# Kernel optimization log

Hardware: AMD Instinct MI355X
Metric: run time of the kernel (lower is better)

Reference implementation:

```python
import jax, jax.numpy as jnp
import numpy as np

N = 1024
B = 32768


def _cc_mul(a, b):
    # complex multiply with real/imag stacked on axis 0; b broadcasts [2,N] against [2,B,N]
    real = a[0] * b[0] - a[1] * b[1]
    imag = a[0] * b[1] + a[1] * b[0]
    return jnp.stack((real, imag), axis=0)


def setup_inputs() -> dict:
    key = jax.random.key(0)
    k1, k2, k3, k4, k5 = jax.random.split(key, 5)
    x = jax.random.normal(k1, (2, B, N), dtype=jnp.float32)
    diag = jax.random.normal(k2, (2, N), dtype=jnp.float32)
    off_diag = jax.random.normal(k3, (2, N), dtype=jnp.float32)
    # pairwise swap permutation: (0,1),(2,3),... swapped -> 1,0,3,2,...
    pairwise = np.arange(N).reshape(-1, 2)[:, ::-1].ravel()
    pairwise_perm_idx = jnp.asarray(pairwise, dtype=jnp.int32)
    left_perm_idx = jax.random.permutation(k4, N).astype(jnp.int32)
    right_perm_idx = jax.random.permutation(k5, N).astype(jnp.int32)
    return {
        "x": x,
        "diag": diag,
        "off_diag": off_diag,
        "pairwise_perm_idx": pairwise_perm_idx,
        "left_perm_idx": left_perm_idx,
        "right_perm_idx": right_perm_idx,
    }


def reference(x, diag, off_diag, pairwise_perm_idx, left_perm_idx, right_perm_idx):
    # left permutation (gather on last dim)
    o = x[..., left_perm_idx]
    # diag path + pairwise-permuted off-diag path (complex MAC)
    out = _cc_mul(o, diag) + _cc_mul(o, off_diag)[..., pairwise_perm_idx]
    # right permutation
    return out[..., right_perm_idx]
```

## Files before the change

### kernel.cpp

```cpp
#include <hip/hip_runtime.h>


#define NCOLS 1024
#define TPB   256
#define KPT   (NCOLS / TPB)
#define BPB   8

__global__ __launch_bounds__(TPB) void mesh_kernel(
    const float* __restrict__ x,
    const float* __restrict__ diag,
    const float* __restrict__ offd,
    const int*   __restrict__ pair,
    const int*   __restrict__ lperm,
    const int*   __restrict__ rperm,
    float* __restrict__ out,
    int B)
{
    __shared__ __align__(16) float smem[2][2 * NCOLS];

    const int t = threadIdx.x;

    int   lr[KPT], lp[KPT];
    float d0[KPT], d1[KPT], f0[KPT], f1[KPT];
#pragma unroll
    for (int k = 0; k < KPT; ++k) {
        int j = t + k * TPB;
        int r = rperm[j];
        int p = pair[r];
        lr[k] = lperm[r];
        lp[k] = lperm[p];
        d0[k] = diag[r];
        d1[k] = diag[NCOLS + r];
        f0[k] = offd[p];
        f1[k] = offd[NCOLS + p];
    }

    const long long BN = (long long)B * NCOLS;
    const int b0 = blockIdx.x * BPB;

    for (int i = 0; i < BPB; ++i) {
        int b = b0 + i;
        if (b >= B) break;
        float* sb = smem[i & 1];

        const float4* r0 = (const float4*)(x + (long long)b * NCOLS);
        const float4* r1 = (const float4*)(x + BN + (long long)b * NCOLS);
        ((float4*)sb)[t]           = r0[t];
        ((float4*)(sb + NCOLS))[t] = r1[t];
        __syncthreads();

#pragma unroll
        for (int k = 0; k < KPT; ++k) {
            float a0 = sb[lr[k]];
            float a1 = sb[NCOLS + lr[k]];
            float e0 = sb[lp[k]];
            float e1 = sb[NCOLS + lp[k]];
            int j = t + k * TPB;
            long long o = (long long)b * NCOLS + j;
            out[o]      = a0 * d0[k] - a1 * d1[k] + e0 * f0[k] - e1 * f1[k];
            out[BN + o] = a0 * d1[k] + a1 * d0[k] + e0 * f1[k] + e1 * f0[k];
        }
    }
}

extern "C" void kernel_launch(void* const* d_in, const int* in_sizes, int n_in,
                              void* d_out, int out_size, void* d_ws, size_t ws_size,
                              hipStream_t stream) {
    const float* x     = (const float*)d_in[0];
    const float* diag  = (const float*)d_in[1];
    const float* offd  = (const float*)d_in[2];
    const int*   pair  = (const int*)d_in[3];
    const int*   lperm = (const int*)d_in[4];
    const int*   rperm = (const int*)d_in[5];
    float* out = (float*)d_out;

    const int N = in_sizes[1] / 2;
    const int B = in_sizes[0] / (2 * N);
    (void)N;

    dim3 grid((B + BPB - 1) / BPB);
    mesh_kernel<<<grid, TPB, 0, stream>>>(x, diag, offd, pair, lperm, rperm, out, B);
}
```

Measured before the change: 444.9 us.

## Prefetch next row into registers and write contiguous float4 outputs per thread

Each thread now owns four contiguous output columns, using the right-permutation indices read as one int4, so results go out as two float4 stores instead of eight scalar stores. The next batch row is loaded from global memory into registers before the current row is computed, then stored into the alternate shared buffer, which overlaps global load latency with compute. Rows per block grow from 8 to 16, which halves the grid and amortises the per-block index and coefficient setup. The costs are higher register pressure and fewer blocks available to hide latency.

```diff
diff --git a/kernel.cpp b/kernel.cpp
--- a/kernel.cpp
+++ b/kernel.cpp
@@ -3,8 +3,9 @@
 
 #define NCOLS 1024
 #define TPB   256
-#define KPT   (NCOLS / TPB)
-#define BPB   8
+#define KPT   4
+#define BPB   16
+#define NBUF  2
 
 __global__ __launch_bounds__(TPB) void mesh_kernel(
     const float* __restrict__ x,
@@ -16,17 +17,18 @@
     float* __restrict__ out,
     int B)
 {
-    __shared__ __align__(16) float smem[2][2 * NCOLS];
+    __shared__ __align__(16) float smem[NBUF][2 * NCOLS];
 
     const int t = threadIdx.x;
 
     int   lr[KPT], lp[KPT];
     float d0[KPT], d1[KPT], f0[KPT], f1[KPT];
+    const int4 rj = ((const int4*)rperm)[t];
+    const int  rr[KPT] = {rj.x, rj.y, rj.z, rj.w};
 #pragma unroll
     for (int k = 0; k < KPT; ++k) {
-        int j = t + k * TPB;
-        int r = rperm[j];
-        int p = pair[r];
+        const int r = rr[k];
+        const int p = pair[r];
         lr[k] = lperm[r];
         lp[k] = lperm[p];
         d0[k] = diag[r];
@@ -37,28 +39,50 @@
 
     const long long BN = (long long)B * NCOLS;
     const int b0 = blockIdx.x * BPB;
+    const int nb = min(BPB, B - b0);
+    if (nb <= 0) return;
 
-    for (int i = 0; i < BPB; ++i) {
-        int b = b0 + i;
-        if (b >= B) break;
-        float* sb = smem[i & 1];
+    const float4* g0 = (const float4*)(x + (long long)b0 * NCOLS);
+    const float4* g1 = (const float4*)(x + BN + (long long)b0 * NCOLS);
+    float* o0p = out + (long long)b0 * NCOLS;
+    float* o1p = o0p + BN;
+    const int RS4 = NCOLS / 4;
 
-        const float4* r0 = (const float4*)(x + (long long)b * NCOLS);
-        const float4* r1 = (const float4*)(x + BN + (long long)b * NCOLS);
-        ((float4*)sb)[t]           = r0[t];
-        ((float4*)(sb + NCOLS))[t] = r1[t];
+    float4 p0 = g0[t];
+    float4 p1 = g1[t];
+    ((float4*)smem[0])[t]           = p0;
+    ((float4*)(smem[0] + NCOLS))[t] = p1;
+
+    for (int i = 0; i < nb; ++i) {
+        const bool pf = (i + 1 < nb);
+
+        if (pf) {
+            p0 = g0[(i + 1) * RS4 + t];
+            p1 = g1[(i + 1) * RS4 + t];
+        }
+
         __syncthreads();
 
+        const float* sb = smem[i & 1];
+        float4 q0, q1;
+        float* q0a = (float*)&q0;
+        float* q1a = (float*)&q1;
 #pragma unroll
         for (int k = 0; k < KPT; ++k) {
-            float a0 = sb[lr[k]];
-            float a1 = sb[NCOLS + lr[k]];
-            float e0 = sb[lp[k]];
-            float e1 = sb[NCOLS + lp[k]];
-            int j = t + k * TPB;
-            long long o = (long long)b * NCOLS + j;
-            out[o]      = a0 * d0[k] - a1 * d1[k] + e0 * f0[k] - e1 * f1[k];
-            out[BN + o] = a0 * d1[k] + a1 * d0[k] + e0 * f1[k] + e1 * f0[k];
+            const float a0 = sb[lr[k]];
+            const float a1 = sb[NCOLS + lr[k]];
+            const float e0 = sb[lp[k]];
+            const float e1 = sb[NCOLS + lp[k]];
+            q0a[k] = a0 * d0[k] - a1 * d1[k] + e0 * f0[k] - e1 * f1[k];
+            q1a[k] = a0 * d1[k] + a1 * d0[k] + e0 * f1[k] + e1 * f0[k];
+        }
+        ((float4*)(o0p + (long long)i * NCOLS))[t] = q0;
+        ((float4*)(o1p + (long long)i * NCOLS))[t] = q1;
+
+        if (pf) {
+            float* nbuf = smem[(i + 1) & 1];
+            ((float4*)nbuf)[t]           = p0;
+            ((float4*)(nbuf + NCOLS))[t] = p1;
         }
     }
 }
```

Measured after the change: 447.0 us. Within noise of the previous version (+0.5%).
